# Kernel tuning notes

Measured on AMD Instinct MI355X. Metric: run time of the kernel, lower is better.

The kernel has to match this reference:

```python
import jax, jax.numpy as jnp
import numpy as np

NUM_CLASSES = 1000
DENSE_DIM = 64 * 64  # 4096, hardcoded in the module
BATCH = 8192
W0, W1 = 0.5, 0.5  # self.weights


def setup_inputs() -> dict:
    key = jax.random.key(0)
    k1, k2, k3, k4 = jax.random.split(key, 4)
    logits = jax.random.normal(k1, (BATCH, NUM_CLASSES), dtype=jnp.float32)
    dense_out = jax.random.normal(k2, (BATCH, DENSE_DIM), dtype=jnp.float32)
    target = jax.random.randint(k3, (BATCH,), 0, NUM_CLASSES, dtype=jnp.int32)
    # dense_labels buffer: random 0/1 per (class, dense) cell, as in __init__
    dense_labels = jax.random.bernoulli(k4, 0.5, (NUM_CLASSES, DENSE_DIM)).astype(jnp.float32)
    return {"logits": logits, "dense_out": dense_out, "target": target,
            "dense_labels": dense_labels}


def _bce_with_logits_mean(x, y):
    # numerically stable BCEWithLogitsLoss (mean reduction)
    return jnp.mean(jnp.maximum(x, 0.0) - x * y + jnp.log1p(jnp.exp(-jnp.abs(x))))


def reference(logits, dense_out, target, dense_labels):
    # --- accumulation (detached in the original; side-effect state) ---
    probs = jax.lax.stop_gradient(jax.nn.sigmoid(dense_out))  # [B, D]
    dense_output_sum = jax.ops.segment_sum(probs, target, num_segments=NUM_CLASSES)  # [C, D]
    total_accumulated = jax.ops.segment_sum(
        jnp.ones((BATCH,), dtype=jnp.float32), target, num_segments=NUM_CLASSES)  # [C]

    # --- losses ---
    dense_target = dense_labels[target]  # per-sample gather of label rows [B, D]
    logp = jax.nn.log_softmax(logits, axis=-1)
    loss1 = -jnp.mean(jnp.take_along_axis(logp, target[:, None], axis=1))  # CrossEntropyLoss
    loss2 = _bce_with_logits_mean(dense_out, dense_target)
    loss = loss1 * W0 + loss2 * W1
    return loss, dense_output_sum, total_accumulated
```

## Files before the change

### kernel.cpp

```cpp
#include <hip/hip_runtime.h>
#include <math.h>

#define NC   1000
#define DD   4096
#define BB   8192

#define MAIN_BLOCKS (NC * 4)
#define CE_BLOCKS   (BB / 4)
#define TOT_BLOCKS  (MAIN_BLOCKS + CE_BLOCKS)
#define MAXN 128
#define NSLOT 32


#define ACC1(xv, yv, acc)                                                     \
    {                                                                         \
        float e = __expf(-fabsf(xv));                                         \
        float inv = __builtin_amdgcn_rcpf(1.f + e);                           \
        acc += (xv >= 0.f) ? inv : e * inv;                                   \
        bce += fmaxf(xv, 0.f) - xv * yv + __logf(1.f + e);                    \
    }

__global__ __launch_bounds__(256) void fused_k(const float* __restrict__ logits,
                                               const float* __restrict__ dense_out,
                                               const int*   __restrict__ target,
                                               const float* __restrict__ dense_labels,
                                               float* __restrict__ out,
                                               double* __restrict__ loss1,
                                               double* __restrict__ loss2) {
    int bx = blockIdx.x;
    int t  = threadIdx.x;
    int wave = t >> 6;
    int lane = t & 63;

    __shared__ int   sidx[MAXN];
    __shared__ int   s_n;
    __shared__ float red[4];

    if (bx < MAIN_BLOCKS) {
        int c     = bx >> 2;
        int chunk = bx & 3;
        int d     = chunk * 1024 + (t << 2);

        if (t == 0) s_n = 0;
        __syncthreads();

        const int4* tp = (const int4*)target;
        #pragma unroll
        for (int k = 0; k < 8; ++k) {
            int4 v = tp[k * 256 + t];
            int s0 = (k * 256 + t) * 4;
            if (v.x == c) { int p = atomicAdd(&s_n, 1); sidx[p] = s0;     }
            if (v.y == c) { int p = atomicAdd(&s_n, 1); sidx[p] = s0 + 1; }
            if (v.z == c) { int p = atomicAdd(&s_n, 1); sidx[p] = s0 + 2; }
            if (v.w == c) { int p = atomicAdd(&s_n, 1); sidx[p] = s0 + 3; }
        }
        __syncthreads();
        int n = s_n;

        float4 y = *(const float4*)(dense_labels + (size_t)c * DD + d);
        float a0 = 0.f, a1 = 0.f, a2 = 0.f, a3 = 0.f, bce = 0.f;
        const float* dp = dense_out + d;

        for (int base = 0; base < n; base += 8) {
            int m = n - base; if (m > 8) m = 8;
            float4 xb[8];
            #pragma unroll
            for (int j = 0; j < 8; ++j)
                if (j < m) xb[j] = *(const float4*)(dp + (size_t)sidx[base + j] * DD);
            #pragma unroll
            for (int j = 0; j < 8; ++j)
                if (j < m) {
                    ACC1(xb[j].x, y.x, a0) ACC1(xb[j].y, y.y, a1)
                    ACC1(xb[j].z, y.z, a2) ACC1(xb[j].w, y.w, a3)
                }
        }

        float* p = out + 1 + (size_t)c * DD + d;
        p[0] = a0; p[1] = a1; p[2] = a2; p[3] = a3;

        if (chunk == 0 && t == 0) out[1 + (size_t)NC * DD + c] = (float)n;

        #pragma unroll
        for (int o2 = 32; o2 > 0; o2 >>= 1) bce += __shfl_xor(bce, o2);
        if (lane == 0) red[wave] = bce;
        __syncthreads();
        if (t == 0)
            atomicAdd(&loss2[bx & (NSLOT - 1)],
                      (double)(red[0] + red[1] + red[2] + red[3]));
    } else {
        int i = (bx - MAIN_BLOCKS) * 4 + wave;
        const float* row = logits + (size_t)i * NC;
        int j0 = lane * 4;

        float4 r0 = *(const float4*)(row + j0);
        float4 r1 = *(const float4*)(row + j0 + 256);
        float4 r2 = *(const float4*)(row + j0 + 512);
        float4 r3;
        if (j0 + 768 < NC) r3 = *(const float4*)(row + j0 + 768);
        else r3 = make_float4(-INFINITY, -INFINITY, -INFINITY, -INFINITY);
        float tl = row[target[i]];

        float mx = fmaxf(fmaxf(fmaxf(r0.x, r0.y), fmaxf(r0.z, r0.w)),
                         fmaxf(fmaxf(r1.x, r1.y), fmaxf(r1.z, r1.w)));
        mx = fmaxf(mx, fmaxf(fmaxf(r2.x, r2.y), fmaxf(r2.z, r2.w)));
        mx = fmaxf(mx, fmaxf(fmaxf(r3.x, r3.y), fmaxf(r3.z, r3.w)));
        #pragma unroll
        for (int o = 32; o > 0; o >>= 1) mx = fmaxf(mx, __shfl_xor(mx, o));

        float s = __expf(r0.x - mx) + __expf(r0.y - mx) + __expf(r0.z - mx) + __expf(r0.w - mx)
                + __expf(r1.x - mx) + __expf(r1.y - mx) + __expf(r1.z - mx) + __expf(r1.w - mx)
                + __expf(r2.x - mx) + __expf(r2.y - mx) + __expf(r2.z - mx) + __expf(r2.w - mx)
                + __expf(r3.x - mx) + __expf(r3.y - mx) + __expf(r3.z - mx) + __expf(r3.w - mx);
        #pragma unroll
        for (int o = 32; o > 0; o >>= 1) s += __shfl_xor(s, o);

        if (lane == 0) red[wave] = -(tl - mx - __logf(s));
        __syncthreads();
        if (t == 0)
            atomicAdd(&loss1[bx & (NSLOT - 1)],
                      (double)(red[0] + red[1] + red[2] + red[3]));
    }
}

__global__ void fin_k(const double* __restrict__ loss1,
                      const double* __restrict__ loss2,
                      float* __restrict__ out) {
    double l1 = 0.0, l2 = 0.0;
    #pragma unroll
    for (int i = 0; i < NSLOT; ++i) { l1 += loss1[i]; l2 += loss2[i]; }
    out[0] = (float)(0.5 * (l1 / (double)BB) +
                     0.5 * (l2 / ((double)BB * (double)DD)));
}

extern "C" void kernel_launch(void* const* d_in, const int* in_sizes, int n_in,
                              void* d_out, int out_size, void* d_ws, size_t ws_size,
                              hipStream_t stream) {
    const float* logits       = (const float*)d_in[0];
    const float* dense_out    = (const float*)d_in[1];
    const int*   target       = (const int*)d_in[2];
    const float* dense_labels = (const float*)d_in[3];
    float* out = (float*)d_out;

    char* ws = (char*)d_ws;
    double* loss1 = (double*)(ws + 0);
    double* loss2 = (double*)(ws + 256);

    hipMemsetAsync(d_ws, 0, 512, stream);

    fused_k<<<TOT_BLOCKS, 256, 0, stream>>>(logits, dense_out, target,
                                            dense_labels, out, loss1, loss2);
    fin_k<<<1, 1, 0, stream>>>(loss1, loss2, out);
}
```

Before: 251.9 us.

## Halve class-chunk blocks, interleave CE blocks, and factor label term out of BCE

```diff
diff --git a/kernel.cpp b/kernel.cpp
--- a/kernel.cpp
+++ b/kernel.cpp
@@ -5,28 +5,32 @@
 #define DD   4096
 #define BB   8192
 
-#define MAIN_BLOCKS (NC * 4)
+#define MAIN_BLOCKS (NC * 2)
 #define CE_BLOCKS   (BB / 4)
 #define TOT_BLOCKS  (MAIN_BLOCKS + CE_BLOCKS)
-#define MAXN 128
+#define MAXN 144
 #define NSLOT 32
+#define LN2  0.69314718055994531f
 
 
-#define ACC1(xv, yv, acc)                                                     \
+#define ACCX(xv, aAcc, sAcc)                                                  \
     {                                                                         \
-        float e = __expf(-fabsf(xv));                                         \
-        float inv = __builtin_amdgcn_rcpf(1.f + e);                           \
-        acc += (xv >= 0.f) ? inv : e * inv;                                   \
-        bce += fmaxf(xv, 0.f) - xv * yv + __logf(1.f + e);                    \
+        float e   = __expf(-fabsf(xv));                                       \
+        float p1  = 1.f + e;                                                  \
+        float inv = __builtin_amdgcn_rcpf(p1);                                \
+        aAcc += (xv >= 0.f) ? inv : e * inv;                                  \
+        sAcc += xv;                                                           \
+        bceA += fmaxf(xv, 0.f);                                               \
+        bceB += __log2f(p1);                                                  \
     }
 
-__global__ __launch_bounds__(256) void fused_k(const float* __restrict__ logits,
-                                               const float* __restrict__ dense_out,
-                                               const int*   __restrict__ target,
-                                               const float* __restrict__ dense_labels,
-                                               float* __restrict__ out,
-                                               double* __restrict__ loss1,
-                                               double* __restrict__ loss2) {
+__global__ __launch_bounds__(256, 4) void fused_k(const float* __restrict__ logits,
+                                                  const float* __restrict__ dense_out,
+                                                  const int*   __restrict__ target,
+                                                  const float* __restrict__ dense_labels,
+                                                  float* __restrict__ out,
+                                                  double* __restrict__ loss1,
+                                                  double* __restrict__ loss2) {
     int bx = blockIdx.x;
     int t  = threadIdx.x;
     int wave = t >> 6;
@@ -36,13 +40,18 @@
     __shared__ int   s_n;
     __shared__ float red[4];
 
-    if (bx < MAIN_BLOCKS) {
-        int c     = bx >> 2;
-        int chunk = bx & 3;
-        int d     = chunk * 1024 + (t << 2);
+    bool is_main = ((bx & 1) == 0) && (bx < 2 * MAIN_BLOCKS);
+
+    if (is_main) {
+        int mb    = bx >> 1;
+        int c     = mb >> 1;
+        int chunk = mb & 1;
+        int dbase = chunk * 2048 + (t << 2);
 
         if (t == 0) s_n = 0;
         __syncthreads();
+
+        const float4* dpA = (const float4*)(dense_out + dbase);
 
         const int4* tp = (const int4*)target;
         #pragma unroll
@@ -55,28 +64,47 @@
             if (v.w == c) { int p = atomicAdd(&s_n, 1); sidx[p] = s0 + 3; }
         }
         __syncthreads();
-        int n = s_n;
+        int n  = s_n;
+        int n2 = (n + 1) & ~1;
+        if (t == 0 && n2 != n) sidx[n] = sidx[0];
+        __syncthreads();
 
-        float4 y = *(const float4*)(dense_labels + (size_t)c * DD + d);
-        float a0 = 0.f, a1 = 0.f, a2 = 0.f, a3 = 0.f, bce = 0.f;
-        const float* dp = dense_out + d;
+        float a0 = 0.f, a1 = 0.f, a2 = 0.f, a3 = 0.f;
+        float a4 = 0.f, a5 = 0.f, a6 = 0.f, a7 = 0.f;
+        float s0 = 0.f, s1 = 0.f, s2 = 0.f, s3 = 0.f;
+        float s4 = 0.f, s5 = 0.f, s6 = 0.f, s7 = 0.f;
+        float bceA = 0.f, bceB = 0.f;
 
-        for (int base = 0; base < n; base += 8) {
-            int m = n - base; if (m > 8) m = 8;
-            float4 xb[8];
-            #pragma unroll
-            for (int j = 0; j < 8; ++j)
-                if (j < m) xb[j] = *(const float4*)(dp + (size_t)sidx[base + j] * DD);
-            #pragma unroll
-            for (int j = 0; j < 8; ++j)
-                if (j < m) {
-                    ACC1(xb[j].x, y.x, a0) ACC1(xb[j].y, y.y, a1)
-                    ACC1(xb[j].z, y.z, a2) ACC1(xb[j].w, y.w, a3)
-                }
+        for (int base = 0; base < n2; base += 2) {
+            int oA = sidx[base]     << 10;
+            int oB = sidx[base + 1] << 10;
+            float4 xa0 = dpA[oA];
+            float4 xa1 = dpA[oA + 256];
+            float4 xb0 = dpA[oB];
+            float4 xb1 = dpA[oB + 256];
+
+            ACCX(xa0.x, a0, s0) ACCX(xa0.y, a1, s1)
+            ACCX(xa0.z, a2, s2) ACCX(xa0.w, a3, s3)
+            ACCX(xa1.x, a4, s4) ACCX(xa1.y, a5, s5)
+            ACCX(xa1.z, a6, s6) ACCX(xa1.w, a7, s7)
+            if (base + 1 < n) {
+                ACCX(xb0.x, a0, s0) ACCX(xb0.y, a1, s1)
+                ACCX(xb0.z, a2, s2) ACCX(xb0.w, a3, s3)
+                ACCX(xb1.x, a4, s4) ACCX(xb1.y, a5, s5)
+                ACCX(xb1.z, a6, s6) ACCX(xb1.w, a7, s7)
+            }
         }
 
-        float* p = out + 1 + (size_t)c * DD + d;
+        const float4* yp = (const float4*)(dense_labels + (size_t)c * DD + dbase);
+        float4 y0 = yp[0];
+        float4 y1 = yp[256];
+        float bce = bceA + LN2 * bceB
+                  - (y0.x * s0 + y0.y * s1 + y0.z * s2 + y0.w * s3
+                   + y1.x * s4 + y1.y * s5 + y1.z * s6 + y1.w * s7);
+
+        float* p = out + 1 + (size_t)c * DD + dbase;
         p[0] = a0; p[1] = a1; p[2] = a2; p[3] = a3;
+        p[1024] = a4; p[1025] = a5; p[1026] = a6; p[1027] = a7;
 
         if (chunk == 0 && t == 0) out[1 + (size_t)NC * DD + c] = (float)n;
 
@@ -85,10 +113,11 @@
         if (lane == 0) red[wave] = bce;
         __syncthreads();
         if (t == 0)
-            atomicAdd(&loss2[bx & (NSLOT - 1)],
+            atomicAdd(&loss2[mb & (NSLOT - 1)],
                       (double)(red[0] + red[1] + red[2] + red[3]));
     } else {
-        int i = (bx - MAIN_BLOCKS) * 4 + wave;
+        int ce_i = (bx < 2 * MAIN_BLOCKS) ? (bx >> 1) : (bx - MAIN_BLOCKS);
+        int i = ce_i * 4 + wave;
         const float* row = logits + (size_t)i * NC;
         int j0 = lane * 4;
 
@@ -117,7 +146,7 @@
         if (lane == 0) red[wave] = -(tl - mx - __logf(s));
         __syncthreads();
         if (t == 0)
-            atomicAdd(&loss1[bx & (NSLOT - 1)],
+            atomicAdd(&loss1[ce_i & (NSLOT - 1)],
                       (double)(red[0] + red[1] + red[2] + red[3]));
     }
 }
```

Measured after the change: 255.9 us. No clear change (+1.6%).
